# Optimization experiments

Hardware: AMD Instinct MI355X
Metric: run time of the kernel (lower is better)

Reference implementation:

```python
import jax, jax.numpy as jnp
import numpy as np
import math

NH = 12      # num attention heads
WIN = 128    # one-sided sliding window
NG = 32      # number of global (prefix) tokens
NEG = -1e9
LN_EPS = 1e-12


def _layernorm(x, g, b):
    mu = jnp.mean(x, axis=-1, keepdims=True)
    var = jnp.mean(jnp.square(x - mu), axis=-1, keepdims=True)
    return (x - mu) * jax.lax.rsqrt(var + LN_EPS) * g + b


def _longformer_self_attn(h, am, Wq, bq, Wk, bk, Wv, bv):
    B, S, D = h.shape
    Dh = D // NH
    w = WIN
    C = S // w  # number of chunks

    def proj(Wm, bm):
        return (h @ Wm + bm).reshape(B, S, NH, Dh).transpose(0, 2, 1, 3)

    q = proj(Wq, bq) * (1.0 / math.sqrt(Dh))  # [B,H,S,Dh]
    k = proj(Wk, bk)
    v = proj(Wv, bv)

    # ---- banded (sliding window) scores, chunked: each query chunk sees 3w keys ----
    kp = jnp.pad(k, ((0, 0), (0, 0), (w, w), (0, 0)))
    vp = jnp.pad(v, ((0, 0), (0, 0), (w, w), (0, 0)))
    idx = jnp.arange(C)[:, None] * w + jnp.arange(3 * w)[None, :]  # [C,3w]
    k3 = kp[:, :, idx]  # [B,H,C,3w,Dh]
    v3 = vp[:, :, idx]
    qc = q.reshape(B, NH, C, w, Dh)
    band = jnp.einsum('bhcqd,bhckd->bhcqk', qc, k3)  # [B,H,C,w,3w]

    qpos = (jnp.arange(C) * w)[:, None, None] + jnp.arange(w)[None, :, None]  # [C,w,1]
    kpos = (idx - w)[:, None, :]  # [C,1,3w] absolute key positions
    valid = (jnp.abs(kpos - qpos) <= w) & (kpos >= NG) & (kpos < S)  # band, exclude global keys

    amp = jnp.pad(am, ((0, 0), (w, w)))
    am3 = amp[:, idx]  # [B,C,3w] additive mask gathered per chunk
    band = band + am3[:, None, :, None, :]
    band = jnp.where(valid[None, None], band, NEG)
    band = band.reshape(B, NH, S, 3 * w)

    # ---- every token also attends to the NG global tokens ----
    gsc = jnp.einsum('bhsd,bhgd->bhsg', q, k[:, :, :NG]) + am[:, None, None, :NG]

    logits = jnp.concatenate([band, gsc], axis=-1)  # [B,H,S,3w+NG]
    probs = jax.nn.softmax(logits, axis=-1)
    pb = probs[..., :3 * w].reshape(B, NH, C, w, 3 * w)
    out = jnp.einsum('bhcqk,bhckd->bhcqd', pb, v3).reshape(B, NH, S, Dh)
    out = out + jnp.einsum('bhsg,bhgd->bhsd', probs[..., 3 * w:], v[:, :, :NG])

    # ---- global tokens attend to everything ----
    gl = jnp.einsum('bhgd,bhsd->bhgs', q[:, :, :NG], k) + am[:, None, None, :]
    outg = jnp.einsum('bhgs,bhsd->bhgd', jax.nn.softmax(gl, axis=-1), v)

    ctx = jnp.concatenate([outg, out[:, :, NG:]], axis=2)  # [B,H,S,Dh]
    return ctx.transpose(0, 2, 1, 3).reshape(B, S, D)


def setup_inputs() -> dict:
    key = jax.random.key(0)
    ks = jax.random.split(key, 8)
    B, S, D, F = 2, 4096, 768, 3072
    p = lambda k_, sh: jax.random.normal(k_, sh, jnp.float32) * 0.02
    return {
        'hidden_states': jax.random.normal(ks[0], (B, S, D), jnp.float32),
        'attention_mask': jnp.zeros((B, S), jnp.float32),
        'Wq': p(ks[1], (D, D)), 'bq': jnp.zeros((D,), jnp.float32),
        'Wk': p(ks[2], (D, D)), 'bk': jnp.zeros((D,), jnp.float32),
        'Wv': p(ks[3], (D, D)), 'bv': jnp.zeros((D,), jnp.float32),
        'Wo': p(ks[4], (D, D)), 'bo': jnp.zeros((D,), jnp.float32),
        'ln1_g': jnp.ones((D,), jnp.float32), 'ln1_b': jnp.zeros((D,), jnp.float32),
        'Wi': p(ks[5], (D, F)), 'bi': jnp.zeros((F,), jnp.float32),
        'Wo2': p(ks[6], (F, D)), 'bo2': jnp.zeros((D,), jnp.float32),
        'ln2_g': jnp.ones((D,), jnp.float32), 'ln2_b': jnp.zeros((D,), jnp.float32),
    }


def reference(hidden_states, attention_mask, Wq, bq, Wk, bk, Wv, bv, Wo, bo,
              ln1_g, ln1_b, Wi, bi, Wo2, bo2, ln2_g, ln2_b):
    ctx = _longformer_self_attn(hidden_states, attention_mask, Wq, bq, Wk, bk, Wv, bv)
    attn_out = _layernorm(ctx @ Wo + bo + hidden_states, ln1_g, ln1_b)
    inter = jax.nn.gelu(attn_out @ Wi + bi, approximate=False)
    layer_out = _layernorm(inter @ Wo2 + bo2 + attn_out, ln2_g, ln2_b)
    return layer_out
```

## Files before the change

kernel.cpp:

```cpp
#include <hip/hip_runtime.h>
#include <math.h>

#define NHEAD 12
#define DH 64
#define S_LEN 4096
#define B_SZ 2
#define D_MODEL 768
#define FF_DIM 3072
#define WINSZ 128
#define NGLB 32
#define NEGV -1e9f
#define NQC 6291456L

typedef __attribute__((ext_vector_type(8))) short bf16x8;
typedef __attribute__((ext_vector_type(4))) float floatx4;

__device__ __forceinline__ unsigned short f2bf(float x) {
    union { float f; unsigned u; } v; v.f = x;
    unsigned r = v.u + 0x7fffu + ((v.u >> 16) & 1u);
    return (unsigned short)(r >> 16);
}
__device__ __forceinline__ float bf2f(unsigned short x) {
    union { unsigned u; float f; } v; v.u = ((unsigned)x) << 16;
    return v.f;
}

__device__ __forceinline__ void async_copy16(const unsigned short* g, unsigned short* l) {
    __builtin_amdgcn_global_load_lds(
        (const __attribute__((address_space(1))) void*)g,
        (__attribute__((address_space(3))) void*)l, 16, 0, 0);
}

__global__ __launch_bounds__(256) void conv_k(
    const float* __restrict__ x, unsigned short* __restrict__ y, long n)
{
    long i = ((long)blockIdx.x * 256 + threadIdx.x) * 4;
    if (i >= n) return;
    float4 v = *(const float4*)(x + i);
    ushort4 o;
    o.x = f2bf(v.x); o.y = f2bf(v.y); o.z = f2bf(v.z); o.w = f2bf(v.w);
    *(ushort4*)(y + i) = o;
}

__global__ __launch_bounds__(256) void bcat_k(
    const float* __restrict__ a, const float* __restrict__ b,
    const float* __restrict__ c, float* __restrict__ o)
{
    int i = blockIdx.x * 256 + threadIdx.x;
    if (i < 768) o[i] = a[i];
    else if (i < 1536) o[i] = b[i - 768];
    else if (i < 2304) o[i] = c[i - 1536];
}

__global__ __launch_bounds__(256) void transpose_k(
    const float* __restrict__ W, unsigned short* __restrict__ WT, int K, int N)
{
    __shared__ float tile[32][33];
    const int tx = threadIdx.x, ty = threadIdx.y;
    const int n0 = blockIdx.x * 32, k0 = blockIdx.y * 32;
#pragma unroll
    for (int i = 0; i < 4; ++i)
        tile[ty + 8 * i][tx] = W[(long)(k0 + ty + 8 * i) * N + n0 + tx];
    __syncthreads();
#pragma unroll
    for (int i = 0; i < 4; ++i)
        WT[(long)(n0 + ty + 8 * i) * K + k0 + tx] = f2bf(tile[tx][ty + 8 * i]);
}

__global__ __launch_bounds__(256) void vt_k(
    const unsigned short* __restrict__ v, unsigned short* __restrict__ vt)
{
    const int bh = blockIdx.y;
    const int s0 = blockIdx.x * 32;
    const int w = threadIdx.x >> 6, lane = threadIdx.x & 63;
    const unsigned short* src = v + ((long)bh * S_LEN + s0 + w * 8) * DH + lane;
    unsigned short r[8];
#pragma unroll
    for (int j = 0; j < 8; ++j) r[j] = src[j * DH];
    unsigned short* dst = vt + ((long)bh * DH + lane) * S_LEN + s0 + w * 8;
    ushort4 lo, hi;
    lo.x = r[0]; lo.y = r[1]; lo.z = r[2]; lo.w = r[3];
    hi.x = r[4]; hi.y = r[5]; hi.z = r[6]; hi.w = r[7];
    *(ushort4*)dst = lo;
    *(ushort4*)(dst + 4) = hi;
}

template <int EPI>
__global__ __launch_bounds__(256) void gemm_bf(
    const unsigned short* __restrict__ A, const unsigned short* __restrict__ BT,
// ... 42 lines not shown
                    af[i], bfr[j], acc[i][j], 0, 0, 0);
        __syncthreads();
    }

    const int col_l = lane & 15, row_l = (lane >> 4) * 4;
#pragma unroll
    for (int i = 0; i < 4; ++i) {
#pragma unroll
        for (int j = 0; j < 4; ++j) {
            const int n = n0 + wc + j * 16 + col_l;
            const float bv = bias[n];
#pragma unroll
            for (int rg = 0; rg < 4; ++rg) {
                const int m = m0 + wr + i * 16 + row_l + rg;
                float v = acc[i][j][rg] + bv;
                if (EPI == 1) {
                    v = 0.5f * v * (1.f + erff(v * 0.70710678118654752f));
                    ((unsigned short*)out)[(long)m * N + n] = f2bf(v);
                } else {
                    const int bb = m >> 12, s = m & 4095;
                    const int part = n / 768;
                    const int nn = n - part * 768;
                    const int hh = nn >> 6, dh = nn & 63;
                    const float sc = (part == 0) ? 0.125f : 1.f;
                    ((unsigned short*)out)[(long)part * NQC +
                        (((long)bb * NHEAD + hh) * S_LEN + s) * DH + dh] = f2bf(v * sc);
                }
            }
        }
    }
}

__global__ __launch_bounds__(256) void gemm_sp(
    const unsigned short* __restrict__ A, const unsigned short* __restrict__ BT,
    float* __restrict__ p0, float* __restrict__ p1,
    int M, int N, int K2, int nx, int ntile)
{
    __shared__ unsigned short As[128 * 32];
    __shared__ unsigned short Bs[128 * 32];
    const int tid = threadIdx.x;
    const int wave = tid >> 6, lane = tid & 63;
    const int t8 = (blockIdx.x & 7) * (gridDim.x >> 3) + (blockIdx.x >> 3);
    const int slice = t8 >= ntile;
    const int tile = t8 - slice * ntile;
    const int m0 = (tile / nx) * 128, n0 = (tile % nx) * 128;
    const int kbeg = slice * K2, kend = kbeg + K2;
    float* P = slice ? p1 : p0;
    const int wr = (wave >> 1) * 64, wc = (wave & 1) * 64;

// ... 27 lines not shown
#pragma unroll
        for (int i = 0; i < 4; ++i)
#pragma unroll
            for (int j = 0; j < 4; ++j)
                acc[i][j] = __builtin_amdgcn_mfma_f32_16x16x32_bf16(
                    af[i], bfr[j], acc[i][j], 0, 0, 0);
        __syncthreads();
    }

    const int col_l = lane & 15, row_l = (lane >> 4) * 4;
#pragma unroll
    for (int i = 0; i < 4; ++i)
#pragma unroll
        for (int j = 0; j < 4; ++j) {
            const int n = n0 + wc + j * 16 + col_l;
#pragma unroll
            for (int rg = 0; rg < 4; ++rg) {
                const int m = m0 + wr + i * 16 + row_l + rg;
                P[(long)m * N + n] = acc[i][j][rg];
            }
        }
}

__global__ __launch_bounds__(256) void band_mfma_k(
    const unsigned short* __restrict__ q, const unsigned short* __restrict__ k,
    const unsigned short* __restrict__ vt, const float* __restrict__ am,
    unsigned short* __restrict__ ctx)
{
    __shared__ unsigned short Ks[32 * 72];
    __shared__ unsigned short Vs[64 * 40];
    __shared__ unsigned short Ps[4][32 * 40];

    const int blk = blockIdx.x;
    const int c = blk & 31;
    const int h = (blk >> 5) % NHEAD;
    const int b = blk / (32 * NHEAD);
    const int tid = threadIdx.x;
    const int wave = tid >> 6, lane = tid & 63;
    const long bh = (long)b * NHEAD + h;

    const unsigned short* kh  = k + bh * S_LEN * DH;
    const unsigned short* vth = vt + bh * (long)DH * S_LEN;
    const float* amb = am + (long)b * S_LEN;

    const int q0 = c * WINSZ + wave * 32;
    const int ln15 = lane & 15, ln4 = lane >> 4;

    bf16x8 qf[2][2];
#pragma unroll
    for (int nt = 0; nt < 2; ++nt)
#pragma unroll
        for (int ks = 0; ks < 2; ++ks)
            qf[nt][ks] = *(const bf16x8*)(q + (bh * S_LEN + q0 + nt * 16 + ln15) * DH
                                          + ks * 32 + ln4 * 8);

    floatx4 o[4][2];
#pragma unroll
    for (int mt = 0; mt < 4; ++mt)
#pragma unroll
        for (int nt = 0; nt < 2; ++nt) o[mt][nt] = (floatx4){0.f, 0.f, 0.f, 0.f};
    float m_r[2] = {-1e30f, -1e30f}, l_r[2] = {0.f, 0.f};

    const int sk_key = tid >> 3, sk_ch = tid & 7;
    const int sv_dim = tid & 63, sv_ch = tid >> 6;
    const bf16x8 zero8 = {0, 0, 0, 0, 0, 0, 0, 0};

    for (int tile = 0; tile < 13; ++tile) {
        const bool glob = (tile == 12);
        const int kbase = glob ? 0 : (c * WINSZ - WINSZ + tile * 32);

        __syncthreads();
        {
            int kpos = kbase + sk_key;
            bf16x8 val = zero8;
            if ((unsigned)kpos < (unsigned)S_LEN)
                val = *(const bf16x8*)(kh + (long)kpos * DH + sk_ch * 8);
            *(bf16x8*)(&Ks[sk_key * 72 + sk_ch * 8]) = val;
        }
        {
            int kc = kbase + sv_ch * 8;
            bf16x8 val = zero8;
            if (kc >= 0 && kc + 8 <= S_LEN)
                val = *(const bf16x8*)(vth + (long)sv_dim * S_LEN + kc);
            *(bf16x8*)(&Vs[sv_dim * 40 + sv_ch * 8]) = val;
        }
        __syncthreads();

        bf16x8 ak[2][2];
#pragma unroll
        for (int mt = 0; mt < 2; ++mt)
#pragma unroll
            for (int ks = 0; ks < 2; ++ks)
                ak[mt][ks] = *(const bf16x8*)(&Ks[(mt * 16 + ln15) * 72 + ks * 32 + ln4 * 8]);

        floatx4 s[2][2];
#pragma unroll
        for (int mt = 0; mt < 2; ++mt)
#pragma unroll
            for (int nt = 0; nt < 2; ++nt) {
                floatx4 acc = (floatx4){0.f, 0.f, 0.f, 0.f};
                acc = __builtin_amdgcn_mfma_f32_16x16x32_bf16(ak[mt][0], qf[nt][0], acc, 0, 0, 0);
                acc = __builtin_amdgcn_mfma_f32_16x16x32_bf16(ak[mt][1], qf[nt][1], acc, 0, 0, 0);
                s[mt][nt] = acc;
            }

#pragma unroll
        for (int mt = 0; mt < 2; ++mt) {
            const int kp0 = kbase + mt * 16 + ln4 * 4;
#pragma unroll
            for (int rg = 0; rg < 4; ++rg) {
                const int kpos = kp0 + rg;
                const bool kin = (unsigned)kpos < (unsigned)S_LEN;
                const float amv = kin ? amb[kpos] : 0.f;
#pragma unroll
                for (int nt = 0; nt < 2; ++nt) {
                    const int qpos = q0 + nt * 16 + ln15;
                    const int dlt = kpos > qpos ? kpos - qpos : qpos - kpos;
                    const bool valid = glob || (kpos >= NGLB && kin && dlt <= WINSZ);
                    s[mt][nt][rg] = valid ? s[mt][nt][rg] + amv : NEGV;
                }
            }
        }

        float alpha[2];
#pragma unroll
        for (int nt = 0; nt < 2; ++nt) {
            float mx = s[0][nt][0];
#pragma unroll
            for (int rg = 1; rg < 4; ++rg) mx = fmaxf(mx, s[0][nt][rg]);
#pragma unroll
            for (int rg = 0; rg < 4; ++rg) mx = fmaxf(mx, s[1][nt][rg]);
            mx = fmaxf(mx, __shfl_xor(mx, 16));
            mx = fmaxf(mx, __shfl_xor(mx, 32));
            const float mn = fmaxf(m_r[nt], mx);
            alpha[nt] = __expf(m_r[nt] - mn);
            m_r[nt] = mn;
        }

#pragma unroll
        for (int nt = 0; nt < 2; ++nt) {
            float sum = 0.f;
#pragma unroll
            for (int mt = 0; mt < 2; ++mt) {
                ushort4 pk;
#pragma unroll
                for (int rg = 0; rg < 4; ++rg) {
                    const float p = __expf(s[mt][nt][rg] - m_r[nt]);
                    sum += p;
                    ((unsigned short*)&pk)[rg] = f2bf(p);
                }
                *(ushort4*)(&Ps[wave][(nt * 16 + ln15) * 40 + mt * 16 + ln4 * 4]) = pk;
            }
            sum += __shfl_xor(sum, 16);
            sum += __shfl_xor(sum, 32);
            l_r[nt] = l_r[nt] * alpha[nt] + sum;
        }

#pragma unroll
        for (int mt = 0; mt < 4; ++mt)
#pragma unroll
            for (int nt = 0; nt < 2; ++nt)
#pragma unroll
                for (int rg = 0; rg < 4; ++rg) o[mt][nt][rg] *= alpha[nt];

        bf16x8 av[4], bp[2];
#pragma unroll
        for (int mt = 0; mt < 4; ++mt)
            av[mt] = *(const bf16x8*)(&Vs[(mt * 16 + ln15) * 40 + ln4 * 8]);
#pragma unroll
        for (int nt = 0; nt < 2; ++nt)
            bp[nt] = *(const bf16x8*)(&Ps[wave][(nt * 16 + ln15) * 40 + ln4 * 8]);
#pragma unroll
        for (int mt = 0; mt < 4; ++mt)
#pragma unroll
            for (int nt = 0; nt < 2; ++nt)
                o[mt][nt] = __builtin_amdgcn_mfma_f32_16x16x32_bf16(
                    av[mt], bp[nt], o[mt][nt], 0, 0, 0);
    }

    const float inv0 = 1.f / l_r[0], inv1 = 1.f / l_r[1];
#pragma unroll
    for (int nt = 0; nt < 2; ++nt) {
        const float inv = nt ? inv1 : inv0;
        const long row = (long)b * S_LEN + q0 + nt * 16 + ln15;
#pragma unroll
        for (int mt = 0; mt < 4; ++mt) {
            ushort4 ov;
#pragma unroll
            for (int rg = 0; rg < 4; ++rg)
                ((unsigned short*)&ov)[rg] = f2bf(o[mt][nt][rg] * inv);
            *(ushort4*)(ctx + row * D_MODEL + h * DH + mt * 16 + ln4 * 4) = ov;
        }
    }
}

__global__ __launch_bounds__(512) void glob_mfma_k(
    const unsigned short* __restrict__ q, const unsigned short* __restrict__ k,
    const unsigned short* __restrict__ vt, const float* __restrict__ am,
    unsigned short* __restrict__ ctx)
{
    __shared__ unsigned short Ps[8][32 * 72];
    __shared__ float Om[64 * 36];
    __shared__ float mW[8][32], lW[8][32], lTot[32];

    const int bh = blockIdx.x;
    const int b = bh / NHEAD, h = bh % NHEAD;
    const int tid = threadIdx.x;
    const int wave = tid >> 6, lane = tid & 63;
    const int ln15 = lane & 15, ln4 = lane >> 4;

    const unsigned short* kh  = k + (long)bh * S_LEN * DH;
    const unsigned short* vth = vt + (long)bh * DH * S_LEN;
    const float* amb = am + (long)b * S_LEN;

    bf16x8 qf[2][2];
#pragma unroll
    for (int nt = 0; nt < 2; ++nt)
#pragma unroll
        for (int ks = 0; ks < 2; ++ks)
            qf[nt][ks] = *(const bf16x8*)(q + ((long)bh * S_LEN + nt * 16 + ln15) * DH
                                          + ks * 32 + ln4 * 8);

    floatx4 o[4][2];
#pragma unroll
    for (int mt = 0; mt < 4; ++mt)
#pragma unroll
        for (int nt = 0; nt < 2; ++nt) o[mt][nt] = (floatx4){0.f, 0.f, 0.f, 0.f};
    float m_r[2] = {-1e30f, -1e30f}, l_r[2] = {0.f, 0.f};

    for (int it = 0; it < 8; ++it) {
        const int kbase = it * 512 + wave * 64;

        bf16x8 ak[4][2];
#pragma unroll
        for (int mt = 0; mt < 4; ++mt)
#pragma unroll
            for (int ks = 0; ks < 2; ++ks)
                ak[mt][ks] = *(const bf16x8*)(kh + (long)(kbase + mt * 16 + ln15) * DH
                                              + ks * 32 + ln4 * 8);

        floatx4 s[4][2];
#pragma unroll
        for (int mt = 0; mt < 4; ++mt)
#pragma unroll
            for (int nt = 0; nt < 2; ++nt) {
                floatx4 acc = (floatx4){0.f, 0.f, 0.f, 0.f};
                acc = __builtin_amdgcn_mfma_f32_16x16x32_bf16(ak[mt][0], qf[nt][0], acc, 0, 0, 0);
                acc = __builtin_amdgcn_mfma_f32_16x16x32_bf16(ak[mt][1], qf[nt][1], acc, 0, 0, 0);
                s[mt][nt] = acc;
            }

#pragma unroll
        for (int mt = 0; mt < 4; ++mt) {
            const int kp0 = kbase + mt * 16 + ln4 * 4;
#pragma unroll
            for (int rg = 0; rg < 4; ++rg) {
                const float amv = amb[kp0 + rg];
#pragma unroll
                for (int nt = 0; nt < 2; ++nt) s[mt][nt][rg] += amv;
            }
        }

        float alpha[2];
#pragma unroll
        for (int nt = 0; nt < 2; ++nt) {
            float mx = s[0][nt][0];
#pragma unroll
            for (int mt = 0; mt < 4; ++mt)
#pragma unroll
                for (int rg = 0; rg < 4; ++rg) mx = fmaxf(mx, s[mt][nt][rg]);
            mx = fmaxf(mx, __shfl_xor(mx, 16));
            mx = fmaxf(mx, __shfl_xor(mx, 32));
            const float mn = fmaxf(m_r[nt], mx);
            alpha[nt] = __expf(m_r[nt] - mn);
            m_r[nt] = mn;
        }

#pragma unroll
        for (int nt = 0; nt < 2; ++nt) {
            float sum = 0.f;
#pragma unroll
            for (int mt = 0; mt < 4; ++mt) {
                ushort4 pk;
#pragma unroll
                for (int rg = 0; rg < 4; ++rg) {
                    const float p = __expf(s[mt][nt][rg] - m_r[nt]);
                    sum += p;
                    ((unsigned short*)&pk)[rg] = f2bf(p);
                }
                *(ushort4*)(&Ps[wave][(nt * 16 + ln15) * 72 + mt * 16 + ln4 * 4]) = pk;
            }
            sum += __shfl_xor(sum, 16);
            sum += __shfl_xor(sum, 32);
            l_r[nt] = l_r[nt] * alpha[nt] + sum;
        }

#pragma unroll
        for (int mt = 0; mt < 4; ++mt)
#pragma unroll
            for (int nt = 0; nt < 2; ++nt)
#pragma unroll
                for (int rg = 0; rg < 4; ++rg) o[mt][nt][rg] *= alpha[nt];

        bf16x8 av[4][2], bp[2][2];
#pragma unroll
        for (int mt = 0; mt < 4; ++mt)
#pragma unroll
            for (int ks = 0; ks < 2; ++ks)
                av[mt][ks] = *(const bf16x8*)(vth + (long)(mt * 16 + ln15) * S_LEN
                                              + kbase + ks * 32 + ln4 * 8);
#pragma unroll
        for (int nt = 0; nt < 2; ++nt)
#pragma unroll
            for (int ks = 0; ks < 2; ++ks)
                bp[nt][ks] = *(const bf16x8*)(&Ps[wave][(nt * 16 + ln15) * 72
                                              + ks * 32 + ln4 * 8]);
#pragma unroll
        for (int mt = 0; mt < 4; ++mt)
#pragma unroll
            for (int nt = 0; nt < 2; ++nt) {
                o[mt][nt] = __builtin_amdgcn_mfma_f32_16x16x32_bf16(
                    av[mt][0], bp[nt][0], o[mt][nt], 0, 0, 0);
                o[mt][nt] = __builtin_amdgcn_mfma_f32_16x16x32_bf16(
                    av[mt][1], bp[nt][1], o[mt][nt], 0, 0, 0);
            }
    }

    if (ln4 == 0) {
#pragma unroll
        for (int nt = 0; nt < 2; ++nt) {
            mW[wave][nt * 16 + ln15] = m_r[nt];
            lW[wave][nt * 16 + ln15] = l_r[nt];
        }
    }
    for (int i = tid; i < 64 * 36; i += 512) Om[i] = 0.f;
    __syncthreads();

    float f[2];
#pragma unroll
    for (int nt = 0; nt < 2; ++nt) {
        const int qq = nt * 16 + ln15;
        float mt_ = mW[0][qq];
#pragma unroll
        for (int w = 1; w < 8; ++w) mt_ = fmaxf(mt_, mW[w][qq]);
        float lt = 0.f;
#pragma unroll
        for (int w = 0; w < 8; ++w) lt += __expf(mW[w][qq] - mt_) * lW[w][qq];
        f[nt] = __expf(m_r[nt] - mt_);
        if (wave == 0 && ln4 == 0) lTot[qq] = lt;
    }
#pragma unroll
    for (int mt = 0; mt < 4; ++mt)
#pragma unroll
        for (int nt = 0; nt < 2; ++nt)
#pragma unroll
            for (int rg = 0; rg < 4; ++rg) o[mt][nt][rg] *= f[nt];

    for (int wv = 0; wv < 8; ++wv) {
        if (wave == wv) {
#pragma unroll
            for (int mt = 0; mt < 4; ++mt)
#pragma unroll
                for (int nt = 0; nt < 2; ++nt)
#pragma unroll
                    for (int rg = 0; rg < 4; ++rg)
                        Om[(mt * 16 + ln4 * 4 + rg) * 36 + nt * 16 + ln15] += o[mt][nt][rg];
        }
        __syncthreads();
    }

    const int qq = tid >> 4, d0 = (tid & 15) * 4;
    const float inv = 1.f / lTot[qq];
    ushort4 ov;
#pragma unroll
    for (int i = 0; i < 4; ++i)
        ((unsigned short*)&ov)[i] = f2bf(Om[(d0 + i) * 36 + qq] * inv);
    *(ushort4*)(ctx + ((long)b * S_LEN + qq) * D_MODEL + h * DH + d0) = ov;
}

__global__ __launch_bounds__(256) void ln2p_k(
    const float* __restrict__ p0, const float* __restrict__ p1,
    const float* __restrict__ bias, const float* __restrict__ resid,
    float* __restrict__ out, unsigned short* __restrict__ out_bf,
    const float* __restrict__ gw, const float* __restrict__ bw)
{
    __shared__ float red[256];
    const long row = blockIdx.x;
    const long base = row * D_MODEL;
    const int t = threadIdx.x;
    float v0 = p0[base + t]       + p1[base + t]       + bias[t]       + resid[base + t];
    float v1 = p0[base + t + 256] + p1[base + t + 256] + bias[t + 256] + resid[base + t + 256];
    float v2 = p0[base + t + 512] + p1[base + t + 512] + bias[t + 512] + resid[base + t + 512];

    red[t] = v0 + v1 + v2;
    __syncthreads();
    for (int off = 128; off; off >>= 1) {
        if (t < off) red[t] += red[t + off];
        __syncthreads();
    }
    const float mu = red[0] * (1.f / 768.f);
    __syncthreads();

    float d0 = v0 - mu, d1 = v1 - mu, d2 = v2 - mu;
    red[t] = d0 * d0 + d1 * d1 + d2 * d2;
    __syncthreads();
    for (int off = 128; off; off >>= 1) {
        if (t < off) red[t] += red[t + off];
        __syncthreads();
    }
    const float var = red[0] * (1.f / 768.f);
    const float rs = rsqrtf(var + 1e-12f);

    const float y0 = d0 * rs * gw[t] + bw[t];
    const float y1 = d1 * rs * gw[t + 256] + bw[t + 256];
    const float y2 = d2 * rs * gw[t + 512] + bw[t + 512];
    if (out) {
        float* y = out + base;
        y[t] = y0; y[t + 256] = y1; y[t + 512] = y2;
    }
    if (out_bf) {
        unsigned short* yb = out_bf + base;
        yb[t] = f2bf(y0); yb[t + 256] = f2bf(y1); yb[t + 512] = f2bf(y2);
    }
}

extern "C" void kernel_launch(void* const* d_in, const int* in_sizes, int n_in,
                              void* d_out, int out_size, void* d_ws, size_t ws_size,
                              hipStream_t stream)
{
    const float* hid  = (const float*)d_in[0];
    const float* am   = (const float*)d_in[1];
    const float* Wq   = (const float*)d_in[2];
    const float* bq   = (const float*)d_in[3];
// ... 18 lines not shown
    unsigned short* W16 = (unsigned short*)d_ws;
    unsigned short* qb   = W16;
    unsigned short* kb   = W16 + NQ;
    unsigned short* vb   = W16 + 2 * NQ;
    unsigned short* vtb  = W16 + 3 * NQ;
    unsigned short* ctxb = W16 + 4 * NQ;
    unsigned short* hidb = W16 + 5 * NQ;
    unsigned short* wqt  = W16 + 6 * NQ;
    unsigned short* wkt  = wqt + 589824;
    unsigned short* wvt  = wkt + 589824;
    unsigned short* wot  = wvt + 589824;
    unsigned short* wit  = wot + 589824;
    unsigned short* wo2t = wit + 2359296;
    float* tmp   = (float*)(W16 + 44826624);
    float* partB1 = (float*)(W16 + 57409536);
    float* bcat  = (float*)(W16 + 69992448);
    float* partA0 = (float*)W16;
    float* partA1 = (float*)(W16 + 2 * NQ);
    unsigned short* interb = W16;
    unsigned short* attnb  = hidb;
    float* partB0 = (float*)(W16 + 4 * NQ);
    (void)ws_size; (void)in_sizes; (void)n_in; (void)out_size;

    transpose_k<<<dim3(24, 24), dim3(32, 8), 0, stream>>>(Wq, wqt, 768, 768);
    transpose_k<<<dim3(24, 24), dim3(32, 8), 0, stream>>>(Wk, wkt, 768, 768);
    transpose_k<<<dim3(24, 24), dim3(32, 8), 0, stream>>>(Wv, wvt, 768, 768);
    transpose_k<<<dim3(24, 24), dim3(32, 8), 0, stream>>>(Wo, wot, 768, 768);
    transpose_k<<<dim3(96, 24), dim3(32, 8), 0, stream>>>(Wi, wit, 768, 3072);
    transpose_k<<<dim3(24, 96), dim3(32, 8), 0, stream>>>(Wo2, wo2t, 3072, 768);
    conv_k<<<dim3((NQ / 4 + 255) / 256), dim3(256), 0, stream>>>(hid, hidb, NQ);
    bcat_k<<<dim3(9), dim3(256), 0, stream>>>(bq, bk, bv, bcat);

    dim3 blk(256);

    gemm_bf<2><<<dim3(1152), blk, 0, stream>>>(hidb, wqt, bcat, qb,
                                               M, 2304, 768, 18);

    vt_k<<<dim3(128, 24), blk, 0, stream>>>(vb, vtb);

    band_mfma_k<<<dim3(768), blk, 0, stream>>>(qb, kb, vtb, am, ctxb);
    glob_mfma_k<<<dim3(B_SZ * NHEAD), dim3(512), 0, stream>>>(qb, kb, vtb, am, ctxb);

    gemm_sp<<<dim3(768), blk, 0, stream>>>(ctxb, wot, partA0, partA1,
                                           M, 768, 384, 6, 384);
    ln2p_k<<<dim3(M), blk, 0, stream>>>(partA0, partA1, bo, hid,
                                        tmp, attnb, ln1g, ln1b);

    gemm_bf<1><<<dim3(1536), blk, 0, stream>>>(attnb, wit, bi, interb,
                                               M, 3072, 768, 24);

    gemm_sp<<<dim3(768), blk, 0, stream>>>(interb, wo2t, partB0, partB1,
                                           M, 768, 1536, 6, 384);
    ln2p_k<<<dim3(M), blk, 0, stream>>>(partB0, partB1, bo2, tmp,
                                        (float*)d_out, nullptr, ln2g, ln2b);
}
```

Measured before the change: 462.9 us.

## Merge prep kernels, fuse band/global attention launch, fold q scale into weights

Combines the six weight transposes, bias concat and hidden conversion into one prep kernel, folding the 1/sqrt(Dh) query scale into Wq and bq. Band and global attention become one launch, with the global blocks now using 4 waves instead of 8. The layernorm reductions switch from shared-memory tree reductions to wave shuffles. The aim is fewer launches and barriers; the global blocks get less parallelism and may become a longer tail.

```diff
diff --git a/kernel.cpp b/kernel.cpp
--- a/kernel.cpp
+++ b/kernel.cpp
@@ -31,40 +31,51 @@
         (__attribute__((address_space(3))) void*)l, 16, 0, 0);
 }
 
-__global__ __launch_bounds__(256) void conv_k(
-    const float* __restrict__ x, unsigned short* __restrict__ y, long n)
-{
-    long i = ((long)blockIdx.x * 256 + threadIdx.x) * 4;
-    if (i >= n) return;
-    float4 v = *(const float4*)(x + i);
-    ushort4 o;
-    o.x = f2bf(v.x); o.y = f2bf(v.y); o.z = f2bf(v.z); o.w = f2bf(v.w);
-    *(ushort4*)(y + i) = o;
-}
-
-__global__ __launch_bounds__(256) void bcat_k(
-    const float* __restrict__ a, const float* __restrict__ b,
-    const float* __restrict__ c, float* __restrict__ o)
-{
-    int i = blockIdx.x * 256 + threadIdx.x;
-    if (i < 768) o[i] = a[i];
-    else if (i < 1536) o[i] = b[i - 768];
-    else if (i < 2304) o[i] = c[i - 1536];
-}
-
-__global__ __launch_bounds__(256) void transpose_k(
-    const float* __restrict__ W, unsigned short* __restrict__ WT, int K, int N)
+__global__ __launch_bounds__(256) void prep_k(
+    const float* __restrict__ Wq, const float* __restrict__ Wk,
+    const float* __restrict__ Wv, const float* __restrict__ Wo,
+    const float* __restrict__ Wi, const float* __restrict__ Wo2,
+    unsigned short* __restrict__ wqt, unsigned short* __restrict__ wkt,
+    unsigned short* __restrict__ wvt, unsigned short* __restrict__ wot,
+    unsigned short* __restrict__ wit, unsigned short* __restrict__ wo2t,
+    const float* __restrict__ bq, const float* __restrict__ bk,
+    const float* __restrict__ bv, float* __restrict__ bcat,
+    const float* __restrict__ hid, unsigned short* __restrict__ hidb)
 {
     __shared__ float tile[32][33];
+    const int bid = blockIdx.x;
     const int tx = threadIdx.x, ty = threadIdx.y;
-    const int n0 = blockIdx.x * 32, k0 = blockIdx.y * 32;
-#pragma unroll
-    for (int i = 0; i < 4; ++i)
-        tile[ty + 8 * i][tx] = W[(long)(k0 + ty + 8 * i) * N + n0 + tx];
-    __syncthreads();
-#pragma unroll
-    for (int i = 0; i < 4; ++i)
-        WT[(long)(n0 + ty + 8 * i) * K + k0 + tx] = f2bf(tile[tx][ty + 8 * i]);
+
+    if (bid < 6912) {
+        const float* src; unsigned short* dst; int K, N, nx, local; float scale = 1.f;
+        if (bid < 576)       { src = Wq;  dst = wqt;  K = 768;  N = 768;  nx = 24; local = bid;        scale = 0.125f; }
+        else if (bid < 1152) { src = Wk;  dst = wkt;  K = 768;  N = 768;  nx = 24; local = bid - 576;  }
+        else if (bid < 1728) { src = Wv;  dst = wvt;  K = 768;  N = 768;  nx = 24; local = bid - 1152; }
+        else if (bid < 2304) { src = Wo;  dst = wot;  K = 768;  N = 768;  nx = 24; local = bid - 1728; }
+        else if (bid < 4608) { src = Wi;  dst = wit;  K = 768;  N = 3072; nx = 96; local = bid - 2304; }
+        else                 { src = Wo2; dst = wo2t; K = 3072; N = 768;  nx = 24; local = bid - 4608; }
+        const int n0 = (local % nx) * 32, k0 = (local / nx) * 32;
+#pragma unroll
+        for (int i = 0; i < 4; ++i)
+            tile[ty + 8 * i][tx] = src[(long)(k0 + ty + 8 * i) * N + n0 + tx];
+        __syncthreads();
+#pragma unroll
+        for (int i = 0; i < 4; ++i)
+            dst[(long)(n0 + ty + 8 * i) * K + k0 + tx] = f2bf(tile[tx][ty + 8 * i] * scale);
+    } else if (bid < 6921) {
+        const int t = ty * 32 + tx;
+        const int i = (bid - 6912) * 256 + t;
+        if (i < 768) bcat[i] = bq[i] * 0.125f;
+        else if (i < 1536) bcat[i] = bk[i - 768];
+        else if (i < 2304) bcat[i] = bv[i - 1536];
+    } else {
+        const int t = ty * 32 + tx;
+        const long i = ((long)(bid - 6921) * 256 + t) * 4;
+        float4 v = *(const float4*)(hid + i);
+        ushort4 o;
+        o.x = f2bf(v.x); o.y = f2bf(v.y); o.z = f2bf(v.z); o.w = f2bf(v.w);
+        *(ushort4*)(hidb + i) = o;
+    }
 }
 
 __global__ __launch_bounds__(256) void vt_k(
@@ -153,9 +164,8 @@
                     const int part = n / 768;
                     const int nn = n - part * 768;
                     const int hh = nn >> 6, dh = nn & 63;
-                    const float sc = (part == 0) ? 0.125f : 1.f;
                     ((unsigned short*)out)[(long)part * NQC +
-                        (((long)bb * NHEAD + hh) * S_LEN + s) * DH + dh] = f2bf(v * sc);
+                        (((long)bb * NHEAD + hh) * S_LEN + s) * DH + dh] = f2bf(v);
                 }
             }
         }
@@ -229,360 +239,365 @@
         }
 }
 
-__global__ __launch_bounds__(256) void band_mfma_k(
+__global__ __launch_bounds__(256) void attn_k(
     const unsigned short* __restrict__ q, const unsigned short* __restrict__ k,
     const unsigned short* __restrict__ vt, const float* __restrict__ am,
     unsigned short* __restrict__ ctx)
 {
-    __shared__ unsigned short Ks[32 * 72];
-    __shared__ unsigned short Vs[64 * 40];
-    __shared__ unsigned short Ps[4][32 * 40];
-
+    __shared__ __align__(16) unsigned char smem[28800];
     const int blk = blockIdx.x;
-    const int c = blk & 31;
-    const int h = (blk >> 5) % NHEAD;
-    const int b = blk / (32 * NHEAD);
-    const int tid = threadIdx.x;
-    const int wave = tid >> 6, lane = tid & 63;
-    const long bh = (long)b * NHEAD + h;
-
-    const unsigned short* kh  = k + bh * S_LEN * DH;
-    const unsigned short* vth = vt + bh * (long)DH * S_LEN;
-    const float* amb = am + (long)b * S_LEN;
-
-    const int q0 = c * WINSZ + wave * 32;
-    const int ln15 = lane & 15, ln4 = lane >> 4;
-
-    bf16x8 qf[2][2];
-#pragma unroll
-    for (int nt = 0; nt < 2; ++nt)
-#pragma unroll
-        for (int ks = 0; ks < 2; ++ks)
-            qf[nt][ks] = *(const bf16x8*)(q + (bh * S_LEN + q0 + nt * 16 + ln15) * DH
-                                          + ks * 32 + ln4 * 8);
-
-    floatx4 o[4][2];
-#pragma unroll
-    for (int mt = 0; mt < 4; ++mt)
-#pragma unroll
-        for (int nt = 0; nt < 2; ++nt) o[mt][nt] = (floatx4){0.f, 0.f, 0.f, 0.f};
-    float m_r[2] = {-1e30f, -1e30f}, l_r[2] = {0.f, 0.f};
-
-    const int sk_key = tid >> 3, sk_ch = tid & 7;
-    const int sv_dim = tid & 63, sv_ch = tid >> 6;
-    const bf16x8 zero8 = {0, 0, 0, 0, 0, 0, 0, 0};
-
-    for (int tile = 0; tile < 13; ++tile) {
-        const bool glob = (tile == 12);
-        const int kbase = glob ? 0 : (c * WINSZ - WINSZ + tile * 32);
-
-        __syncthreads();
-        {
-            int kpos = kbase + sk_key;
-            bf16x8 val = zero8;
-            if ((unsigned)kpos < (unsigned)S_LEN)
-                val = *(const bf16x8*)(kh + (long)kpos * DH + sk_ch * 8);
-            *(bf16x8*)(&Ks[sk_key * 72 + sk_ch * 8]) = val;
-        }
-        {
-            int kc = kbase + sv_ch * 8;
-            bf16x8 val = zero8;
-            if (kc >= 0 && kc + 8 <= S_LEN)
-                val = *(const bf16x8*)(vth + (long)sv_dim * S_LEN + kc);
-            *(bf16x8*)(&Vs[sv_dim * 40 + sv_ch * 8]) = val;
-        }
-        __syncthreads();
-
-        bf16x8 ak[2][2];
-#pragma unroll
-        for (int mt = 0; mt < 2; ++mt)
-#pragma unroll
-            for (int ks = 0; ks < 2; ++ks)
-                ak[mt][ks] = *(const bf16x8*)(&Ks[(mt * 16 + ln15) * 72 + ks * 32 + ln4 * 8]);
-
-        floatx4 s[2][2];
-#pragma unroll
-        for (int mt = 0; mt < 2; ++mt)
-#pragma unroll
-            for (int nt = 0; nt < 2; ++nt) {
-                floatx4 acc = (floatx4){0.f, 0.f, 0.f, 0.f};
-                acc = __builtin_amdgcn_mfma_f32_16x16x32_bf16(ak[mt][0], qf[nt][0], acc, 0, 0, 0);
-                acc = __builtin_amdgcn_mfma_f32_16x16x32_bf16(ak[mt][1], qf[nt][1], acc, 0, 0, 0);
-                s[mt][nt] = acc;
-            }
-
-#pragma unroll
-        for (int mt = 0; mt < 2; ++mt) {
-            const int kp0 = kbase + mt * 16 + ln4 * 4;
-#pragma unroll
-            for (int rg = 0; rg < 4; ++rg) {
-                const int kpos = kp0 + rg;
-                const bool kin = (unsigned)kpos < (unsigned)S_LEN;
-                const float amv = kin ? amb[kpos] : 0.f;
-#pragma unroll
-                for (int nt = 0; nt < 2; ++nt) {
-                    const int qpos = q0 + nt * 16 + ln15;
-                    const int dlt = kpos > qpos ? kpos - qpos : qpos - kpos;
-                    const bool valid = glob || (kpos >= NGLB && kin && dlt <= WINSZ);
-                    s[mt][nt][rg] = valid ? s[mt][nt][rg] + amv : NEGV;
-                }
-            }
-        }
-
-        float alpha[2];
-#pragma unroll
-        for (int nt = 0; nt < 2; ++nt) {
-            float mx = s[0][nt][0];
-#pragma unroll
-            for (int rg = 1; rg < 4; ++rg) mx = fmaxf(mx, s[0][nt][rg]);
-#pragma unroll
-            for (int rg = 0; rg < 4; ++rg) mx = fmaxf(mx, s[1][nt][rg]);
-            mx = fmaxf(mx, __shfl_xor(mx, 16));
-            mx = fmaxf(mx, __shfl_xor(mx, 32));
-            const float mn = fmaxf(m_r[nt], mx);
-            alpha[nt] = __expf(m_r[nt] - mn);
-            m_r[nt] = mn;
-        }
-
-#pragma unroll
-        for (int nt = 0; nt < 2; ++nt) {
-            float sum = 0.f;
-#pragma unroll
-            for (int mt = 0; mt < 2; ++mt) {
-                ushort4 pk;
-#pragma unroll
-                for (int rg = 0; rg < 4; ++rg) {
-                    const float p = __expf(s[mt][nt][rg] - m_r[nt]);
-                    sum += p;
-                    ((unsigned short*)&pk)[rg] = f2bf(p);
-                }
-                *(ushort4*)(&Ps[wave][(nt * 16 + ln15) * 40 + mt * 16 + ln4 * 4]) = pk;
-            }
-            sum += __shfl_xor(sum, 16);
-            sum += __shfl_xor(sum, 32);
-            l_r[nt] = l_r[nt] * alpha[nt] + sum;
-        }
-
-#pragma unroll
-        for (int mt = 0; mt < 4; ++mt)
-#pragma unroll
-            for (int nt = 0; nt < 2; ++nt)
-#pragma unroll
-                for (int rg = 0; rg < 4; ++rg) o[mt][nt][rg] *= alpha[nt];
-
-        bf16x8 av[4], bp[2];
-#pragma unroll
-        for (int mt = 0; mt < 4; ++mt)
-            av[mt] = *(const bf16x8*)(&Vs[(mt * 16 + ln15) * 40 + ln4 * 8]);
-#pragma unroll
-        for (int nt = 0; nt < 2; ++nt)
-            bp[nt] = *(const bf16x8*)(&Ps[wave][(nt * 16 + ln15) * 40 + ln4 * 8]);
-#pragma unroll
-        for (int mt = 0; mt < 4; ++mt)
-#pragma unroll
-            for (int nt = 0; nt < 2; ++nt)
-                o[mt][nt] = __builtin_amdgcn_mfma_f32_16x16x32_bf16(
-                    av[mt], bp[nt], o[mt][nt], 0, 0, 0);
-    }
-
-    const float inv0 = 1.f / l_r[0], inv1 = 1.f / l_r[1];
-#pragma unroll
-    for (int nt = 0; nt < 2; ++nt) {
-        const float inv = nt ? inv1 : inv0;
-        const long row = (long)b * S_LEN + q0 + nt * 16 + ln15;
-#pragma unroll
-        for (int mt = 0; mt < 4; ++mt) {
-            ushort4 ov;
-#pragma unroll
-            for (int rg = 0; rg < 4; ++rg)
-                ((unsigned short*)&ov)[rg] = f2bf(o[mt][nt][rg] * inv);
-            *(ushort4*)(ctx + row * D_MODEL + h * DH + mt * 16 + ln4 * 4) = ov;
-        }
-    }
-}
-
-__global__ __launch_bounds__(512) void glob_mfma_k(
-    const unsigned short* __restrict__ q, const unsigned short* __restrict__ k,
-    const unsigned short* __restrict__ vt, const float* __restrict__ am,
-    unsigned short* __restrict__ ctx)
-{
-    __shared__ unsigned short Ps[8][32 * 72];
-    __shared__ float Om[64 * 36];
-    __shared__ float mW[8][32], lW[8][32], lTot[32];
-
-    const int bh = blockIdx.x;
-    const int b = bh / NHEAD, h = bh % NHEAD;
     const int tid = threadIdx.x;
     const int wave = tid >> 6, lane = tid & 63;
     const int ln15 = lane & 15, ln4 = lane >> 4;
 
-    const unsigned short* kh  = k + (long)bh * S_LEN * DH;
-    const unsigned short* vth = vt + (long)bh * DH * S_LEN;
-    const float* amb = am + (long)b * S_LEN;
-
-    bf16x8 qf[2][2];
-#pragma unroll
-    for (int nt = 0; nt < 2; ++nt)
-#pragma unroll
-        for (int ks = 0; ks < 2; ++ks)
-            qf[nt][ks] = *(const bf16x8*)(q + ((long)bh * S_LEN + nt * 16 + ln15) * DH
-                                          + ks * 32 + ln4 * 8);
-
-    floatx4 o[4][2];
-#pragma unroll
-    for (int mt = 0; mt < 4; ++mt)
-#pragma unroll
-        for (int nt = 0; nt < 2; ++nt) o[mt][nt] = (floatx4){0.f, 0.f, 0.f, 0.f};
-    float m_r[2] = {-1e30f, -1e30f}, l_r[2] = {0.f, 0.f};
-
-    for (int it = 0; it < 8; ++it) {
-        const int kbase = it * 512 + wave * 64;
-
-        bf16x8 ak[4][2];
+    if (blk >= 24) {
+        unsigned short* Ks = (unsigned short*)smem;
+        unsigned short* Vs = Ks + 32 * 72;
+        unsigned short* Ps = Vs + 64 * 40;
+
+        const int bb = blk - 24;
+        const int c = bb & 31;
+        const int h = (bb >> 5) % NHEAD;
+        const int b = bb / (32 * NHEAD);
+        const long bh = (long)b * NHEAD + h;
+
+        const unsigned short* kh  = k + bh * S_LEN * DH;
+        const unsigned short* vth = vt + bh * (long)DH * S_LEN;
+        const float* amb = am + (long)b * S_LEN;
+
+        const int q0 = c * WINSZ + wave * 32;
+
+        bf16x8 qf[2][2];
+#pragma unroll
+        for (int nt = 0; nt < 2; ++nt)
+#pragma unroll
+            for (int ks = 0; ks < 2; ++ks)
+                qf[nt][ks] = *(const bf16x8*)(q + (bh * S_LEN + q0 + nt * 16 + ln15) * DH
+                                              + ks * 32 + ln4 * 8);
+
+        floatx4 o[4][2];
 #pragma unroll
         for (int mt = 0; mt < 4; ++mt)
 #pragma unroll
+            for (int nt = 0; nt < 2; ++nt) o[mt][nt] = (floatx4){0.f, 0.f, 0.f, 0.f};
+        float m_r[2] = {-1e30f, -1e30f}, l_r[2] = {0.f, 0.f};
+
+        const int sk_key = tid >> 3, sk_ch = tid & 7;
+        const int sv_dim = tid & 63, sv_ch = tid >> 6;
+        const bf16x8 zero8 = {0, 0, 0, 0, 0, 0, 0, 0};
+
+        for (int tile = 0; tile < 13; ++tile) {
+            const bool glob = (tile == 12);
+            const int kbase = glob ? 0 : (c * WINSZ - WINSZ + tile * 32);
+
+            __syncthreads();
+            {
+                int kpos = kbase + sk_key;
+                bf16x8 val = zero8;
+                if ((unsigned)kpos < (unsigned)S_LEN)
+                    val = *(const bf16x8*)(kh + (long)kpos * DH + sk_ch * 8);
+                *(bf16x8*)(&Ks[sk_key * 72 + sk_ch * 8]) = val;
+            }
+            {
+                int kc = kbase + sv_ch * 8;
+                bf16x8 val = zero8;
+                if (kc >= 0 && kc + 8 <= S_LEN)
+                    val = *(const bf16x8*)(vth + (long)sv_dim * S_LEN + kc);
+                *(bf16x8*)(&Vs[sv_dim * 40 + sv_ch * 8]) = val;
+            }
+            __syncthreads();
+
+            bf16x8 ak[2][2];
+#pragma unroll
+            for (int mt = 0; mt < 2; ++mt)
+#pragma unroll
+                for (int ks = 0; ks < 2; ++ks)
+                    ak[mt][ks] = *(const bf16x8*)(&Ks[(mt * 16 + ln15) * 72 + ks * 32 + ln4 * 8]);
+
+            floatx4 s[2][2];
+#pragma unroll
+            for (int mt = 0; mt < 2; ++mt)
+#pragma unroll
+                for (int nt = 0; nt < 2; ++nt) {
+                    floatx4 acc = (floatx4){0.f, 0.f, 0.f, 0.f};
+                    acc = __builtin_amdgcn_mfma_f32_16x16x32_bf16(ak[mt][0], qf[nt][0], acc, 0, 0, 0);
+                    acc = __builtin_amdgcn_mfma_f32_16x16x32_bf16(ak[mt][1], qf[nt][1], acc, 0, 0, 0);
+                    s[mt][nt] = acc;
+                }
+
+#pragma unroll
+            for (int mt = 0; mt < 2; ++mt) {
+                const int kp0 = kbase + mt * 16 + ln4 * 4;
+#pragma unroll
+                for (int rg = 0; rg < 4; ++rg) {
+                    const int kpos = kp0 + rg;
+                    const bool kin = (unsigned)kpos < (unsigned)S_LEN;
+                    const float amv = kin ? amb[kpos] : 0.f;
+#pragma unroll
+                    for (int nt = 0; nt < 2; ++nt) {
+                        const int qpos = q0 + nt * 16 + ln15;
+                        const int dlt = kpos > qpos ? kpos - qpos : qpos - kpos;
+                        const bool valid = glob || (kpos >= NGLB && kin && dlt <= WINSZ);
+                        s[mt][nt][rg] = valid ? s[mt][nt][rg] + amv : NEGV;
+                    }
+                }
+            }
+
+            float alpha[2];
+#pragma unroll
+            for (int nt = 0; nt < 2; ++nt) {
+                float mx = s[0][nt][0];
+#pragma unroll
+                for (int rg = 1; rg < 4; ++rg) mx = fmaxf(mx, s[0][nt][rg]);
+#pragma unroll
+                for (int rg = 0; rg < 4; ++rg) mx = fmaxf(mx, s[1][nt][rg]);
+                mx = fmaxf(mx, __shfl_xor(mx, 16));
+                mx = fmaxf(mx, __shfl_xor(mx, 32));
+                const float mn = fmaxf(m_r[nt], mx);
+                alpha[nt] = __expf(m_r[nt] - mn);
+                m_r[nt] = mn;
+            }
+
+#pragma unroll
+            for (int nt = 0; nt < 2; ++nt) {
+                float sum = 0.f;
+#pragma unroll
+                for (int mt = 0; mt < 2; ++mt) {
+                    ushort4 pk;
+#pragma unroll
+                    for (int rg = 0; rg < 4; ++rg) {
+                        const float p = __expf(s[mt][nt][rg] - m_r[nt]);
+                        sum += p;
+                        ((unsigned short*)&pk)[rg] = f2bf(p);
+                    }
+                    *(ushort4*)(&Ps[wave * 1280 + (nt * 16 + ln15) * 40 + mt * 16 + ln4 * 4]) = pk;
+                }
+                sum += __shfl_xor(sum, 16);
+                sum += __shfl_xor(sum, 32);
+                l_r[nt] = l_r[nt] * alpha[nt] + sum;
+            }
+
+#pragma unroll
+            for (int mt = 0; mt < 4; ++mt)
+#pragma unroll
+                for (int nt = 0; nt < 2; ++nt)
+#pragma unroll
+                    for (int rg = 0; rg < 4; ++rg) o[mt][nt][rg] *= alpha[nt];
+
+            bf16x8 av[4], bp[2];
+#pragma unroll
+            for (int mt = 0; mt < 4; ++mt)
+                av[mt] = *(const bf16x8*)(&Vs[(mt * 16 + ln15) * 40 + ln4 * 8]);
+#pragma unroll
+            for (int nt = 0; nt < 2; ++nt)
+                bp[nt] = *(const bf16x8*)(&Ps[wave * 1280 + (nt * 16 + ln15) * 40 + ln4 * 8]);
+#pragma unroll
+            for (int mt = 0; mt < 4; ++mt)
+#pragma unroll
+                for (int nt = 0; nt < 2; ++nt)
+                    o[mt][nt] = __builtin_amdgcn_mfma_f32_16x16x32_bf16(
+                        av[mt], bp[nt], o[mt][nt], 0, 0, 0);
+        }
+
+        if (q0 >= NGLB) {
+            const float inv0 = 1.f / l_r[0], inv1 = 1.f / l_r[1];
+#pragma unroll
+            for (int nt = 0; nt < 2; ++nt) {
+                const float inv = nt ? inv1 : inv0;
+                const long row = (long)b * S_LEN + q0 + nt * 16 + ln15;
+#pragma unroll
+                for (int mt = 0; mt < 4; ++mt) {
+                    ushort4 ov;
+#pragma unroll
+                    for (int rg = 0; rg < 4; ++rg)
+                        ((unsigned short*)&ov)[rg] = f2bf(o[mt][nt][rg] * inv);
+                    *(ushort4*)(ctx + row * D_MODEL + h * DH + mt * 16 + ln4 * 4) = ov;
+                }
+            }
+        }
+    } else {
+        unsigned short* Psg = (unsigned short*)smem;
+        float* Om   = (float*)(smem + 18432);
+        float* mW   = (float*)(smem + 27648);
+        float* lW   = (float*)(smem + 28160);
+        float* lTot = (float*)(smem + 28672);
+
+        const int bh = blk;
+        const int b = bh / NHEAD, h = bh % NHEAD;
+
+        const unsigned short* kh  = k + (long)bh * S_LEN * DH;
+        const unsigned short* vth = vt + (long)bh * DH * S_LEN;
+        const float* amb = am + (long)b * S_LEN;
+
+        bf16x8 qf[2][2];
+#pragma unroll
+        for (int nt = 0; nt < 2; ++nt)
+#pragma unroll
             for (int ks = 0; ks < 2; ++ks)
-                ak[mt][ks] = *(const bf16x8*)(kh + (long)(kbase + mt * 16 + ln15) * DH
+                qf[nt][ks] = *(const bf16x8*)(q + ((long)bh * S_LEN + nt * 16 + ln15) * DH
                                               + ks * 32 + ln4 * 8);
 
-        floatx4 s[4][2];
+        floatx4 o[4][2];
 #pragma unroll
         for (int mt = 0; mt < 4; ++mt)
 #pragma unroll
+            for (int nt = 0; nt < 2; ++nt) o[mt][nt] = (floatx4){0.f, 0.f, 0.f, 0.f};
+        float m_r[2] = {-1e30f, -1e30f}, l_r[2] = {0.f, 0.f};
+
+        for (int it = 0; it < 16; ++it) {
+            const int kbase = it * 256 + wave * 64;
+
+            bf16x8 ak[4][2];
+#pragma unroll
+            for (int mt = 0; mt < 4; ++mt)
+#pragma unroll
+                for (int ks = 0; ks < 2; ++ks)
+                    ak[mt][ks] = *(const bf16x8*)(kh + (long)(kbase + mt * 16 + ln15) * DH
+                                                  + ks * 32 + ln4 * 8);
+
+            floatx4 s[4][2];
+#pragma unroll
+            for (int mt = 0; mt < 4; ++mt)
+#pragma unroll
+                for (int nt = 0; nt < 2; ++nt) {
+                    floatx4 acc = (floatx4){0.f, 0.f, 0.f, 0.f};
+                    acc = __builtin_amdgcn_mfma_f32_16x16x32_bf16(ak[mt][0], qf[nt][0], acc, 0, 0, 0);
+                    acc = __builtin_amdgcn_mfma_f32_16x16x32_bf16(ak[mt][1], qf[nt][1], acc, 0, 0, 0);
+                    s[mt][nt] = acc;
+                }
+
+#pragma unroll
+            for (int mt = 0; mt < 4; ++mt) {
+                const int kp0 = kbase + mt * 16 + ln4 * 4;
+#pragma unroll
+                for (int rg = 0; rg < 4; ++rg) {
+                    const float amv = amb[kp0 + rg];
+#pragma unroll
+                    for (int nt = 0; nt < 2; ++nt) s[mt][nt][rg] += amv;
+                }
+            }
+
+            float alpha[2];
+#pragma unroll
             for (int nt = 0; nt < 2; ++nt) {
-                floatx4 acc = (floatx4){0.f, 0.f, 0.f, 0.f};
-                acc = __builtin_amdgcn_mfma_f32_16x16x32_bf16(ak[mt][0], qf[nt][0], acc, 0, 0, 0);
-                acc = __builtin_amdgcn_mfma_f32_16x16x32_bf16(ak[mt][1], qf[nt][1], acc, 0, 0, 0);
-                s[mt][nt] = acc;
-            }
-
-#pragma unroll
-        for (int mt = 0; mt < 4; ++mt) {
-            const int kp0 = kbase + mt * 16 + ln4 * 4;
-#pragma unroll
-            for (int rg = 0; rg < 4; ++rg) {
-                const float amv = amb[kp0 + rg];
-#pragma unroll
-                for (int nt = 0; nt < 2; ++nt) s[mt][nt][rg] += amv;
-            }
-        }
-
-        float alpha[2];
+                float mx = s[0][nt][0];
+#pragma unroll
+                for (int mt = 0; mt < 4; ++mt)
+#pragma unroll
+                    for (int rg = 0; rg < 4; ++rg) mx = fmaxf(mx, s[mt][nt][rg]);
+                mx = fmaxf(mx, __shfl_xor(mx, 16));
+                mx = fmaxf(mx, __shfl_xor(mx, 32));
+                const float mn = fmaxf(m_r[nt], mx);
+                alpha[nt] = __expf(m_r[nt] - mn);
+                m_r[nt] = mn;
+            }
+
+#pragma unroll
+            for (int nt = 0; nt < 2; ++nt) {
+                float sum = 0.f;
+#pragma unroll
+                for (int mt = 0; mt < 4; ++mt) {
+                    ushort4 pk;
+#pragma unroll
+                    for (int rg = 0; rg < 4; ++rg) {
+                        const float p = __expf(s[mt][nt][rg] - m_r[nt]);
+                        sum += p;
+                        ((unsigned short*)&pk)[rg] = f2bf(p);
+                    }
+                    *(ushort4*)(&Psg[wave * 2304 + (nt * 16 + ln15) * 72 + mt * 16 + ln4 * 4]) = pk;
+                }
+                sum += __shfl_xor(sum, 16);
+                sum += __shfl_xor(sum, 32);
+                l_r[nt] = l_r[nt] * alpha[nt] + sum;
+            }
+
+#pragma unroll
+            for (int mt = 0; mt < 4; ++mt)
+#pragma unroll
+                for (int nt = 0; nt < 2; ++nt)
+#pragma unroll
+                    for (int rg = 0; rg < 4; ++rg) o[mt][nt][rg] *= alpha[nt];
+
+            bf16x8 av[4][2], bp[2][2];
+#pragma unroll
+            for (int mt = 0; mt < 4; ++mt)
+#pragma unroll
+                for (int ks = 0; ks < 2; ++ks)
+                    av[mt][ks] = *(const bf16x8*)(vth + (long)(mt * 16 + ln15) * S_LEN
+                                                  + kbase + ks * 32 + ln4 * 8);
+#pragma unroll
+            for (int nt = 0; nt < 2; ++nt)
+#pragma unroll
+                for (int ks = 0; ks < 2; ++ks)
+                    bp[nt][ks] = *(const bf16x8*)(&Psg[wave * 2304 + (nt * 16 + ln15) * 72
+                                                  + ks * 32 + ln4 * 8]);
+#pragma unroll
+            for (int mt = 0; mt < 4; ++mt)
+#pragma unroll
+                for (int nt = 0; nt < 2; ++nt) {
+                    o[mt][nt] = __builtin_amdgcn_mfma_f32_16x16x32_bf16(
+                        av[mt][0], bp[nt][0], o[mt][nt], 0, 0, 0);
+                    o[mt][nt] = __builtin_amdgcn_mfma_f32_16x16x32_bf16(
+                        av[mt][1], bp[nt][1], o[mt][nt], 0, 0, 0);
+                }
+        }
+
+        if (ln4 == 0) {
+#pragma unroll
+            for (int nt = 0; nt < 2; ++nt) {
+                mW[wave * 32 + nt * 16 + ln15] = m_r[nt];
+                lW[wave * 32 + nt * 16 + ln15] = l_r[nt];
+            }
+        }
+        for (int i = tid; i < 64 * 36; i += 256) Om[i] = 0.f;
+        __syncthreads();
+
+        float f[2];
 #pragma unroll
         for (int nt = 0; nt < 2; ++nt) {
-            float mx = s[0][nt][0];
-#pragma unroll
-            for (int mt = 0; mt < 4; ++mt)
-#pragma unroll
-                for (int rg = 0; rg < 4; ++rg) mx = fmaxf(mx, s[mt][nt][rg]);
-            mx = fmaxf(mx, __shfl_xor(mx, 16));
-            mx = fmaxf(mx, __shfl_xor(mx, 32));
-            const float mn = fmaxf(m_r[nt], mx);
-            alpha[nt] = __expf(m_r[nt] - mn);
-            m_r[nt] = mn;
-        }
-
-#pragma unroll
-        for (int nt = 0; nt < 2; ++nt) {
-            float sum = 0.f;
-#pragma unroll
-            for (int mt = 0; mt < 4; ++mt) {
-                ushort4 pk;
-#pragma unroll
-                for (int rg = 0; rg < 4; ++rg) {
-                    const float p = __expf(s[mt][nt][rg] - m_r[nt]);
-                    sum += p;
-                    ((unsigned short*)&pk)[rg] = f2bf(p);
-                }
-                *(ushort4*)(&Ps[wave][(nt * 16 + ln15) * 72 + mt * 16 + ln4 * 4]) = pk;
-            }
-            sum += __shfl_xor(sum, 16);
-            sum += __shfl_xor(sum, 32);
-            l_r[nt] = l_r[nt] * alpha[nt] + sum;
-        }
-
+            const int qq = nt * 16 + ln15;
+            float mt_ = mW[qq];
+#pragma unroll
+            for (int w = 1; w < 4; ++w) mt_ = fmaxf(mt_, mW[w * 32 + qq]);
+            float lt = 0.f;
+#pragma unroll
+            for (int w = 0; w < 4; ++w) lt += __expf(mW[w * 32 + qq] - mt_) * lW[w * 32 + qq];
+            f[nt] = __expf(m_r[nt] - mt_);
+            if (wave == 0 && ln4 == 0) lTot[qq] = lt;
+        }
 #pragma unroll
         for (int mt = 0; mt < 4; ++mt)
 #pragma unroll
             for (int nt = 0; nt < 2; ++nt)
 #pragma unroll
-                for (int rg = 0; rg < 4; ++rg) o[mt][nt][rg] *= alpha[nt];
-
-        bf16x8 av[4][2], bp[2][2];
-#pragma unroll
-        for (int mt = 0; mt < 4; ++mt)
-#pragma unroll
-            for (int ks = 0; ks < 2; ++ks)
-                av[mt][ks] = *(const bf16x8*)(vth + (long)(mt * 16 + ln15) * S_LEN
-                                              + kbase + ks * 32 + ln4 * 8);
-#pragma unroll
-        for (int nt = 0; nt < 2; ++nt)
-#pragma unroll
-            for (int ks = 0; ks < 2; ++ks)
-                bp[nt][ks] = *(const bf16x8*)(&Ps[wave][(nt * 16 + ln15) * 72
-                                              + ks * 32 + ln4 * 8]);
-#pragma unroll
-        for (int mt = 0; mt < 4; ++mt)
-#pragma unroll
-            for (int nt = 0; nt < 2; ++nt) {
-                o[mt][nt] = __builtin_amdgcn_mfma_f32_16x16x32_bf16(
-                    av[mt][0], bp[nt][0], o[mt][nt], 0, 0, 0);
-                o[mt][nt] = __builtin_amdgcn_mfma_f32_16x16x32_bf16(
-                    av[mt][1], bp[nt][1], o[mt][nt], 0, 0, 0);
-            }
+                for (int rg = 0; rg < 4; ++rg) o[mt][nt][rg] *= f[nt];
+
+        for (int wv = 0; wv < 4; ++wv) {
+            if (wave == wv) {
+#pragma unroll
+                for (int mt = 0; mt < 4; ++mt)
+#pragma unroll
+                    for (int nt = 0; nt < 2; ++nt)
+#pragma unroll
+                        for (int rg = 0; rg < 4; ++rg)
+                            Om[(mt * 16 + ln4 * 4 + rg) * 36 + nt * 16 + ln15] += o[mt][nt][rg];
+            }
+            __syncthreads();
+        }
+
+        const int qq = tid >> 3, d0 = (tid & 7) * 8;
+        const float inv = 1.f / lTot[qq];
+        ushort4 ov0, ov1;
+#pragma unroll
+        for (int i = 0; i < 4; ++i)
+            ((unsigned short*)&ov0)[i] = f2bf(Om[(d0 + i) * 36 + qq] * inv);
+#pragma unroll
+        for (int i = 0; i < 4; ++i)
+            ((unsigned short*)&ov1)[i] = f2bf(Om[(d0 + 4 + i) * 36 + qq] * inv);
+        unsigned short* dst = ctx + ((long)b * S_LEN + qq) * D_MODEL + h * DH + d0;
+        *(ushort4*)dst = ov0;
+        *(ushort4*)(dst + 4) = ov1;
     }
-
-    if (ln4 == 0) {
-#pragma unroll
-        for (int nt = 0; nt < 2; ++nt) {
-            mW[wave][nt * 16 + ln15] = m_r[nt];
-            lW[wave][nt * 16 + ln15] = l_r[nt];
-        }
-    }
-    for (int i = tid; i < 64 * 36; i += 512) Om[i] = 0.f;
-    __syncthreads();
-
-    float f[2];
-#pragma unroll
-    for (int nt = 0; nt < 2; ++nt) {
-        const int qq = nt * 16 + ln15;
-        float mt_ = mW[0][qq];
-#pragma unroll
-        for (int w = 1; w < 8; ++w) mt_ = fmaxf(mt_, mW[w][qq]);
-        float lt = 0.f;
-#pragma unroll
-        for (int w = 0; w < 8; ++w) lt += __expf(mW[w][qq] - mt_) * lW[w][qq];
-        f[nt] = __expf(m_r[nt] - mt_);
-        if (wave == 0 && ln4 == 0) lTot[qq] = lt;
-    }
-#pragma unroll
-    for (int mt = 0; mt < 4; ++mt)
-#pragma unroll
-        for (int nt = 0; nt < 2; ++nt)
-#pragma unroll
-            for (int rg = 0; rg < 4; ++rg) o[mt][nt][rg] *= f[nt];
-
-    for (int wv = 0; wv < 8; ++wv) {
-        if (wave == wv) {
-#pragma unroll
-            for (int mt = 0; mt < 4; ++mt)
-#pragma unroll
-                for (int nt = 0; nt < 2; ++nt)
-#pragma unroll
-                    for (int rg = 0; rg < 4; ++rg)
-                        Om[(mt * 16 + ln4 * 4 + rg) * 36 + nt * 16 + ln15] += o[mt][nt][rg];
-        }
-        __syncthreads();
-    }
-
-    const int qq = tid >> 4, d0 = (tid & 15) * 4;
-    const float inv = 1.f / lTot[qq];
-    ushort4 ov;
-#pragma unroll
-    for (int i = 0; i < 4; ++i)
-        ((unsigned short*)&ov)[i] = f2bf(Om[(d0 + i) * 36 + qq] * inv);
-    *(ushort4*)(ctx + ((long)b * S_LEN + qq) * D_MODEL + h * DH + d0) = ov;
 }
 
 __global__ __launch_bounds__(256) void ln2p_k(
@@ -591,31 +606,28 @@
     float* __restrict__ out, unsigned short* __restrict__ out_bf,
     const float* __restrict__ gw, const float* __restrict__ bw)
 {
-    __shared__ float red[256];
-    const long row = blockIdx.x;
-    const long base = row * D_MODEL;
+    __shared__ float red[8];
+    const long base = (long)blockIdx.x * D_MODEL;
     const int t = threadIdx.x;
+    const int wv = t >> 6, lane = t & 63;
     float v0 = p0[base + t]       + p1[base + t]       + bias[t]       + resid[base + t];
     float v1 = p0[base + t + 256] + p1[base + t + 256] + bias[t + 256] + resid[base + t + 256];
     float v2 = p0[base + t + 512] + p1[base + t + 512] + bias[t + 512] + resid[base + t + 512];
 
-    red[t] = v0 + v1 + v2;
+    float s = v0 + v1 + v2;
+#pragma unroll
+    for (int off = 32; off; off >>= 1) s += __shfl_xor(s, off);
+    if (lane == 0) red[wv] = s;
     __syncthreads();
-    for (int off = 128; off; off >>= 1) {
-        if (t < off) red[t] += red[t + off];
-        __syncthreads();
-    }
-    const float mu = red[0] * (1.f / 768.f);
+    const float mu = (red[0] + red[1] + red[2] + red[3]) * (1.f / 768.f);
+
+    const float d0 = v0 - mu, d1 = v1 - mu, d2 = v2 - mu;
+    float s2 = d0 * d0 + d1 * d1 + d2 * d2;
+#pragma unroll
+    for (int off = 32; off; off >>= 1) s2 += __shfl_xor(s2, off);
+    if (lane == 0) red[4 + wv] = s2;
     __syncthreads();
-
-    float d0 = v0 - mu, d1 = v1 - mu, d2 = v2 - mu;
-    red[t] = d0 * d0 + d1 * d1 + d2 * d2;
-    __syncthreads();
-    for (int off = 128; off; off >>= 1) {
-        if (t < off) red[t] += red[t + off];
-        __syncthreads();
-    }
-    const float var = red[0] * (1.f / 768.f);
+    const float var = (red[4] + red[5] + red[6] + red[7]) * (1.f / 768.f);
     const float rs = rsqrtf(var + 1e-12f);
 
     const float y0 = d0 * rs * gw[t] + bw[t];
@@ -680,14 +692,9 @@
     float* partB0 = (float*)(W16 + 4 * NQ);
     (void)ws_size; (void)in_sizes; (void)n_in; (void)out_size;
 
-    transpose_k<<<dim3(24, 24), dim3(32, 8), 0, stream>>>(Wq, wqt, 768, 768);
-    transpose_k<<<dim3(24, 24), dim3(32, 8), 0, stream>>>(Wk, wkt, 768, 768);
-    transpose_k<<<dim3(24, 24), dim3(32, 8), 0, stream>>>(Wv, wvt, 768, 768);
-    transpose_k<<<dim3(24, 24), dim3(32, 8), 0, stream>>>(Wo, wot, 768, 768);
-    transpose_k<<<dim3(96, 24), dim3(32, 8), 0, stream>>>(Wi, wit, 768, 3072);
-    transpose_k<<<dim3(24, 96), dim3(32, 8), 0, stream>>>(Wo2, wo2t, 3072, 768);
-    conv_k<<<dim3((NQ / 4 + 255) / 256), dim3(256), 0, stream>>>(hid, hidb, NQ);
-    bcat_k<<<dim3(9), dim3(256), 0, stream>>>(bq, bk, bv, bcat);
+    prep_k<<<dim3(13065), dim3(32, 8), 0, stream>>>(
+        Wq, Wk, Wv, Wo, Wi, Wo2, wqt, wkt, wvt, wot, wit, wo2t,
+        bq, bk, bv, bcat, hid, hidb);
 
     dim3 blk(256);
 
@@ -696,8 +703,7 @@
 
     vt_k<<<dim3(128, 24), blk, 0, stream>>>(vb, vtb);
 
-    band_mfma_k<<<dim3(768), blk, 0, stream>>>(qb, kb, vtb, am, ctxb);
-    glob_mfma_k<<<dim3(B_SZ * NHEAD), dim3(512), 0, stream>>>(qb, kb, vtb, am, ctxb);
+    attn_k<<<dim3(792), blk, 0, stream>>>(qb, kb, vtb, am, ctxb);
 
     gemm_sp<<<dim3(768), blk, 0, stream>>>(ctxb, wot, partA0, partA1,
                                            M, 768, 384, 6, 384);
```

After: 422.0 us. -8.8%, faster.
